# Kernel tuning notes

Measured on AMD Instinct MI355X. Metric: run time of the kernel, lower is better.

The kernel has to match this reference:

```python
import jax, jax.numpy as jnp
import numpy as np

D_MAX = 50


def setup_inputs() -> dict:
    key = jax.random.key(0)
    k1, k2, k3 = jax.random.split(key, 3)
    B, T, P, Q = 16, D_MAX + 1, 2048, 2048
    buf = jax.random.uniform(k1, (B, T, P), dtype=jnp.float32)
    weight = jax.random.normal(k2, (P, Q), dtype=jnp.float32) * np.sqrt(2.0 / P)
    delay_raw = jax.random.normal(k3, (P, Q), dtype=jnp.float32)
    return {"buf": buf, "weight": weight, "delay_raw": delay_raw}


def reference(buf, weight, delay_raw):
    # buf: [B, T, P], weight/delay_raw: [P, Q]
    d_cont = D_MAX * jax.nn.sigmoid(delay_raw)                      # [P, Q] in [0, d_max]
    d_floor = jnp.clip(jnp.floor(d_cont), 0, D_MAX).astype(jnp.int32)
    d_ceil = jnp.clip(d_floor + 1, 0, D_MAX)
    alpha = d_cont - d_floor.astype(d_cont.dtype)                   # [P, Q]

    buf_t = jnp.transpose(buf, (0, 2, 1))                           # [B, P, T]
    # per-synapse gather: s_f[b,p,q] = buf[b, d_floor[p,q], p]
    s_f = jnp.take_along_axis(buf_t, d_floor[None, :, :], axis=2)   # [B, P, Q]
    s_c = jnp.take_along_axis(buf_t, d_ceil[None, :, :], axis=2)    # [B, P, Q]
    s = (1.0 - alpha) * s_f + alpha * s_c                           # [B, P, Q]
    # weighted reduce over pre-neurons
    return jnp.einsum('bpq,pq->bq', s, weight)                      # [B, Q]
```

## Files before the change

### kernel.cpp

```cpp
#include <hip/hip_runtime.h>

#define D_MAX   50
#define T_DIM   51
#define B_DIM   16
#define P_DIM   2048
#define Q_DIM   2048
#define TSTRIDE 80
#define PBY     4112
#define PSPAN   32
#define NPBLK   (P_DIM / PSPAN)
#define QB      512
#define PCHK    8


__device__ __forceinline__ float dot2bf(unsigned taps, unsigned cw, float acc) {
    float d;
    asm("v_dot2_f32_bf16 %0, %1, %2, %3" : "=v"(d) : "v"(taps), "v"(cw), "v"(acc));
    return d;
}
__device__ __forceinline__ unsigned pack_bf16x2(float lo, float hi) {
    unsigned r;
    asm("v_cvt_pk_bf16_f32 %0, %1, %2" : "=v"(r) : "v"(lo), "v"(hi));
    return r;
}
__device__ __forceinline__ unsigned short rne_bf16(float v) {
    unsigned x = __float_as_uint(v);
    x += 0x7fffu + ((x >> 16) & 1u);
    return (unsigned short)(x >> 16);
}

#define PREFETCH(wArr, xArr, cc)                                            \
    _Pragma("unroll")                                                       \
    for (int j = 0; j < PCHK; ++j) {                                        \
        wArr[j] = Wq[(size_t)(p0 + (cc) * PCHK + j) * Q_DIM];               \
        xArr[j] = Dq[(size_t)(p0 + (cc) * PCHK + j) * Q_DIM];               \
    }

#define COMPUTE8(wArr, xArr, cc)                                            \
    _Pragma("unroll")                                                       \
    for (int jj = 0; jj < PCHK; ++jj) {                                     \
        const int p = (cc) * PCHK + jj;                                     \
        const float w = wArr[jj], x = xArr[jj];                             \
        const float d = 50.f / (1.f + __expf(-x));                          \
        const int df = min((int)d, D_MAX);                                  \
        const float a  = d - (float)df;                                     \
        const float wa = w * a;                                             \
        const unsigned cw = pack_bf16x2(w - wa, wa);                        \
        const char* rb = lds + p * PBY + df * TSTRIDE;                      \
        const uint4 u0 = *(const uint4*)(rb);                               \
        const uint4 u1 = *(const uint4*)(rb + 16);                          \
        const uint4 u2 = *(const uint4*)(rb + 32);                          \
        const uint4 u3 = *(const uint4*)(rb + 48);                          \
        acc[0]  = dot2bf(u0.x, cw, acc[0]);                                 \
        acc[1]  = dot2bf(u0.y, cw, acc[1]);                                 \
        acc[2]  = dot2bf(u0.z, cw, acc[2]);                                 \
        acc[3]  = dot2bf(u0.w, cw, acc[3]);                                 \
        acc[4]  = dot2bf(u1.x, cw, acc[4]);                                 \
        acc[5]  = dot2bf(u1.y, cw, acc[5]);                                 \
        acc[6]  = dot2bf(u1.z, cw, acc[6]);                                 \
        acc[7]  = dot2bf(u1.w, cw, acc[7]);                                 \
        acc[8]  = dot2bf(u2.x, cw, acc[8]);                                 \
        acc[9]  = dot2bf(u2.y, cw, acc[9]);                                 \
        acc[10] = dot2bf(u2.z, cw, acc[10]);                                \
        acc[11] = dot2bf(u2.w, cw, acc[11]);                                \
        acc[12] = dot2bf(u3.x, cw, acc[12]);                                \
        acc[13] = dot2bf(u3.y, cw, acc[13]);                                \
        acc[14] = dot2bf(u3.z, cw, acc[14]);                                \
        acc[15] = dot2bf(u3.w, cw, acc[15]);                                \
    }

__global__ __launch_bounds__(512, 2) void dsl_fused_kernel(
    const float* __restrict__ buf, const float* __restrict__ W,
    const float* __restrict__ DR, unsigned short* __restrict__ partial) {
    __shared__ char lds[PSPAN * PBY];
    const int tid = threadIdx.x;
    const int i  = blockIdx.x;
    const int xq = i >> 6;
    const int yp = ((i & 7) << 3) | ((i >> 3) & 7);
    const int q  = xq * QB + tid;
    const int p0 = yp * PSPAN;

    {
        const int bb = tid >> 5, pl = tid & 31;
        const float* src = buf + (size_t)bb * (T_DIM * P_DIM) + p0 + pl;
        float v[T_DIM + 1];
#pragma unroll
        for (int t = 0; t < T_DIM; ++t)
            v[t] = src[(size_t)t * P_DIM];
        v[T_DIM] = 0.f;
        char* wb = lds + pl * PBY + bb * 4;
#pragma unroll
        for (int t = 0; t < T_DIM; ++t)
            *(unsigned*)(wb + t * TSTRIDE) = pack_bf16x2(v[t], v[t + 1]);
    }

    const float* Wq = W + q;
    const float* Dq = DR + q;
    float wA[PCHK], xA[PCHK], wB[PCHK], xB[PCHK];
    PREFETCH(wA, xA, 0)
    __syncthreads();

    float acc[B_DIM];
#pragma unroll
    for (int b = 0; b < B_DIM; ++b) acc[b] = 0.f;

    PREFETCH(wB, xB, 1)
    COMPUTE8(wA, xA, 0)
    PREFETCH(wA, xA, 2)
    COMPUTE8(wB, xB, 1)
    PREFETCH(wB, xB, 3)
    COMPUTE8(wA, xA, 2)
    COMPUTE8(wB, xB, 3)

    unsigned short* dst = partial + (size_t)yp * (B_DIM * Q_DIM) + q;
#pragma unroll
    for (int b = 0; b < B_DIM; ++b)
        dst[(size_t)b * Q_DIM] = rne_bf16(acc[b]);
}

__global__ __launch_bounds__(256) void dsl_reduce_kernel(
    const unsigned short* __restrict__ partial, float* __restrict__ out) {
    __shared__ float lds[4][64];
    const int j = threadIdx.x & 63, w = threadIdx.x >> 6;
    const int idx = blockIdx.x * 64 + j;
    float s = 0.f;
    for (int c = w; c < NPBLK; c += 4) {
        const unsigned u = partial[(size_t)c * (B_DIM * Q_DIM) + idx];
        s += __uint_as_float(u << 16);
    }
    lds[w][j] = s;
    __syncthreads();
    if (w == 0)
        out[idx] = lds[0][j] + lds[1][j] + lds[2][j] + lds[3][j];
}

extern "C" void kernel_launch(void* const* d_in, const int* in_sizes, int n_in,
                              void* d_out, int out_size, void* d_ws, size_t ws_size,
                              hipStream_t stream) {
    const float* buf = (const float*)d_in[0];
    const float* W   = (const float*)d_in[1];
    const float* DR  = (const float*)d_in[2];
    float* out = (float*)d_out;

    unsigned short* partial = (unsigned short*)d_ws;

    hipLaunchKernelGGL(dsl_fused_kernel, dim3(256), dim3(512), 0, stream,
                       buf, W, DR, partial);
    hipLaunchKernelGGL(dsl_reduce_kernel, dim3((B_DIM * Q_DIM) / 64), dim3(256), 0, stream,
                       partial, out);
}
```

Baseline: 21.47 us.

## Fuse reduction into main kernel via cooperative grid sync

Replaces the separate reduce kernel launch with a cooperative launch: after writing bf16 partials, each block waits on a grid-wide barrier, then reduces a 128-element slice of the output across all 64 P-blocks. This removes the second kernel launch and its gap. In exchange it adds a grid sync, which has its own cost and requires all 256 blocks to be co-resident (512 threads, ~128KB LDS, 2 per CU on 256 CUs).

```diff
diff --git a/kernel.cpp b/kernel.cpp
--- a/kernel.cpp
+++ b/kernel.cpp
@@ -1,4 +1,7 @@
 #include <hip/hip_runtime.h>
+#include <hip/hip_cooperative_groups.h>
+
+namespace cg = cooperative_groups;
 
 #define D_MAX   50
 #define T_DIM   51
@@ -71,7 +74,8 @@
 
 __global__ __launch_bounds__(512, 2) void dsl_fused_kernel(
     const float* __restrict__ buf, const float* __restrict__ W,
-    const float* __restrict__ DR, unsigned short* __restrict__ partial) {
+    const float* __restrict__ DR, unsigned short* __restrict__ partial,
+    float* __restrict__ out) {
     __shared__ char lds[PSPAN * PBY];
     const int tid = threadIdx.x;
     const int i  = blockIdx.x;
@@ -116,22 +120,22 @@
 #pragma unroll
     for (int b = 0; b < B_DIM; ++b)
         dst[(size_t)b * Q_DIM] = rne_bf16(acc[b]);
-}
 
-__global__ __launch_bounds__(256) void dsl_reduce_kernel(
-    const unsigned short* __restrict__ partial, float* __restrict__ out) {
-    __shared__ float lds[4][64];
-    const int j = threadIdx.x & 63, w = threadIdx.x >> 6;
-    const int idx = blockIdx.x * 64 + j;
+    cg::this_grid().sync();
+
+    const int o0 = i * 128;
+    const int oo = tid & 127, cgi = tid >> 7;
     float s = 0.f;
-    for (int c = w; c < NPBLK; c += 4) {
-        const unsigned u = partial[(size_t)c * (B_DIM * Q_DIM) + idx];
+#pragma unroll 4
+    for (int c = cgi; c < NPBLK; c += 4) {
+        const unsigned u = partial[(size_t)c * (B_DIM * Q_DIM) + o0 + oo];
         s += __uint_as_float(u << 16);
     }
-    lds[w][j] = s;
+    float* red = (float*)lds;
+    red[cgi * 128 + oo] = s;
     __syncthreads();
-    if (w == 0)
-        out[idx] = lds[0][j] + lds[1][j] + lds[2][j] + lds[3][j];
+    if (tid < 128)
+        out[o0 + tid] = red[tid] + red[128 + tid] + red[256 + tid] + red[384 + tid];
 }
 
 extern "C" void kernel_launch(void* const* d_in, const int* in_sizes, int n_in,
@@ -144,8 +148,7 @@
 
     unsigned short* partial = (unsigned short*)d_ws;
 
-    hipLaunchKernelGGL(dsl_fused_kernel, dim3(256), dim3(512), 0, stream,
-                       buf, W, DR, partial);
-    hipLaunchKernelGGL(dsl_reduce_kernel, dim3((B_DIM * Q_DIM) / 64), dim3(256), 0, stream,
-                       partial, out);
+    void* args[] = {(void*)&buf, (void*)&W, (void*)&DR, (void*)&partial, (void*)&out};
+    hipLaunchCooperativeKernel((const void*)dsl_fused_kernel, dim3(256), dim3(512),
+                               args, 0, stream);
 }
```

New measurement: 55.42 us. 2.58x slower.
